# Performance work log

Hardware: AMD Instinct MI355X
Metric: run time of the kernel (lower is better)

The kernel has to match this reference:

```python
import jax, jax.numpy as jnp
import numpy as np

D_MODEL = 256
NUM_HEADS = 8
NUM_KV_HEADS = 4
HEAD_DIM = D_MODEL // NUM_HEADS
EPS = 1e-5


def layer_norm(x, g, b):
    mu = jnp.mean(x, axis=-1, keepdims=True)
    var = jnp.var(x, axis=-1, keepdims=True)
    return (x - mu) * jax.lax.rsqrt(var + EPS) * g + b


def gqa(x_q, x_kv, Wq, bq, Wk, bk, Wv, bv, Wo, bo):
    # x_q, x_kv: [BC, S, D]
    BC, S, D = x_q.shape
    G = NUM_HEADS // NUM_KV_HEADS
    q = (x_q @ Wq + bq).reshape(BC, S, NUM_HEADS, HEAD_DIM)
    k = (x_kv @ Wk + bk).reshape(BC, S, NUM_KV_HEADS, HEAD_DIM)
    v = (x_kv @ Wv + bv).reshape(BC, S, NUM_KV_HEADS, HEAD_DIM)
    # repeat_interleave over head dim to expand KV heads to query heads
    k = jnp.repeat(k, G, axis=2)
    v = jnp.repeat(v, G, axis=2)
    scale = 1.0 / np.sqrt(HEAD_DIM).astype(np.float32)
    scores = jnp.einsum('bqhd,bkhd->bhqk', q, k) * scale  # [BC,H,S,S]
    attn = jax.nn.softmax(scores, axis=-1)
    out = jnp.einsum('bhqk,bkhd->bqhd', attn, v).reshape(BC, S, D)
    return out @ Wo + bo


def _make_params(key):
    ks = jax.random.split(key, 20)
    D, Dkv = D_MODEL, NUM_KV_HEADS * HEAD_DIM
    s = 1.0 / np.sqrt(D).astype(np.float32)
    p = {}
    # 4 LayerNorms
    for name in ['spec_q', 'spec_kv', 'spat_q', 'spat_kv']:
        p[f'ln_{name}_g'] = jnp.ones((D,), jnp.float32)
        p[f'ln_{name}_b'] = jnp.zeros((D,), jnp.float32)
    # two GQA modules: s2t and t2s
    i = 0
    for tag in ['s2t', 't2s']:
        p[f'Wq_{tag}'] = jax.random.normal(ks[i], (D, D), jnp.float32) * s; i += 1
        p[f'bq_{tag}'] = jnp.zeros((D,), jnp.float32)
        p[f'Wk_{tag}'] = jax.random.normal(ks[i], (D, Dkv), jnp.float32) * s; i += 1
        p[f'bk_{tag}'] = jnp.zeros((Dkv,), jnp.float32)
        p[f'Wv_{tag}'] = jax.random.normal(ks[i], (D, Dkv), jnp.float32) * s; i += 1
        p[f'bv_{tag}'] = jnp.zeros((Dkv,), jnp.float32)
        p[f'Wo_{tag}'] = jax.random.normal(ks[i], (D, D), jnp.float32) * s; i += 1
        p[f'bo_{tag}'] = jnp.zeros((D,), jnp.float32)
    p['gate_spec'] = jnp.zeros((1,), jnp.float32)
    p['gate_spat'] = jnp.zeros((1,), jnp.float32)
    return p


def setup_inputs() -> dict:
    key = jax.random.key(0)
    k1, k2, k3 = jax.random.split(key, 3)
    B, S, C, D = 8, 64, 128, D_MODEL
    inp = {
        'x_spec': jax.random.normal(k1, (B, S, C, D), jnp.float32),
        'x_spat': jax.random.normal(k2, (B, S, C, D), jnp.float32),
    }
    inp.update(_make_params(k3))
    return inp


def reference(x_spec, x_spat,
              ln_spec_q_g, ln_spec_q_b, ln_spec_kv_g, ln_spec_kv_b,
              ln_spat_q_g, ln_spat_q_b, ln_spat_kv_g, ln_spat_kv_b,
              Wq_s2t, bq_s2t, Wk_s2t, bk_s2t, Wv_s2t, bv_s2t, Wo_s2t, bo_s2t,
              Wq_t2s, bq_t2s, Wk_t2s, bk_t2s, Wv_t2s, bv_t2s, Wo_t2s, bo_t2s,
              gate_spec, gate_spat):
    B, S, C, D = x_spec.shape
    # (B,S,C,D) -> (B*C, S, D)
    spec_flat = jnp.transpose(x_spec, (0, 2, 1, 3)).reshape(B * C, S, D)
    spat_flat = jnp.transpose(x_spat, (0, 2, 1, 3)).reshape(B * C, S, D)

    spec_q = layer_norm(spec_flat, ln_spec_q_g, ln_spec_q_b)
    spat_kv = layer_norm(spat_flat, ln_spat_kv_g, ln_spat_kv_b)
    delta_spec = gqa(spec_q, spat_kv, Wq_s2t, bq_s2t, Wk_s2t, bk_s2t, Wv_s2t, bv_s2t, Wo_s2t, bo_s2t)

    spat_q = layer_norm(spat_flat, ln_spat_q_g, ln_spat_q_b)
    spec_kv = layer_norm(spec_flat, ln_spec_kv_g, ln_spec_kv_b)
    delta_spat = gqa(spat_q, spec_kv, Wq_t2s, bq_t2s, Wk_t2s, bk_t2s, Wv_t2s, bv_t2s, Wo_t2s, bo_t2s)

    delta_spec = jnp.transpose(delta_spec.reshape(B, C, S, D), (0, 2, 1, 3))
    delta_spat = jnp.transpose(delta_spat.reshape(B, C, S, D), (0, 2, 1, 3))

    out_spec = x_spec + jax.nn.sigmoid(gate_spec) * delta_spec
    out_spat = x_spat + jax.nn.sigmoid(gate_spat) * delta_spat
    return (out_spec, out_spat)
```

## Files before the change

kernel.cpp:

```cpp
#include <hip/hip_runtime.h>

typedef short short8 __attribute__((ext_vector_type(8)));
typedef float f32x4 __attribute__((ext_vector_type(4)));

#define NELT 16777216

__device__ __forceinline__ float b2f(unsigned short u) {
    return __uint_as_float(((unsigned)u) << 16);
}
__device__ __forceinline__ unsigned short f2b(float f) {
    unsigned u = __float_as_uint(f);
    u += 0x7FFF + ((u >> 16) & 1);
    return (unsigned short)(u >> 16);
}
__device__ __forceinline__ void split2(float f, unsigned short& hi, unsigned short& lo) {
    unsigned short h = f2b(f);
    hi = h;
    lo = f2b(f - b2f(h));
}
__device__ __forceinline__ int xrow_off(int r) {
    int n = r >> 6, s = r & 63;
    int b = n >> 7, c = n & 127;
    return (((b << 6) + s) * 128 + c) << 8;
}
__device__ __forceinline__ int sw256(int row, int k) {
    return row * 256 + ((((k >> 3) ^ (row & 7)) << 3) | (k & 7));
}
__device__ __forceinline__ int boff(int nt, int kk, int ct, int lq, int lm) {
    return ((((nt * 8 + kk) * 4 + ct) * 4 + lq) * 16 + lm) * 16;
}

__global__ __launch_bounds__(256) void w_prep(
    const float* __restrict__ Wq, const float* __restrict__ Wk,
    const float* __restrict__ Wv, const float* __restrict__ Wo,
    unsigned short* __restrict__ Bqkv, unsigned short* __restrict__ Bo)
{
    const int tid = blockIdx.x * 256 + threadIdx.x;
    const int lm = tid & 15, lq = (tid >> 4) & 3, ct = (tid >> 6) & 3;
    const int kk = (tid >> 8) & 7, nt = tid >> 11;
    const int c = ct * 16 + lm;
    {
        const float* W; int ldw, col;
        if (nt < 4)      { W = Wq; ldw = 256; col = nt * 64 + c; }
        else if (nt < 6) { W = Wk; ldw = 128; col = (nt - 4) * 64 + c; }
        else             { W = Wv; ldw = 128; col = (nt - 6) * 64 + c; }
        short8 h8, l8;
        #pragma unroll
        for (int j = 0; j < 8; ++j) {
            int k = kk * 32 + lq * 8 + j;
            unsigned short h, l;
            split2(W[k * ldw + col], h, l);
            h8[j] = (short)h; l8[j] = (short)l;
        }
        int off = boff(nt, kk, ct, lq, lm);
        *(short8*)&Bqkv[off] = h8;
        *(short8*)&Bqkv[off + 8] = l8;
    }
    if (nt < 4) {
        int col = nt * 64 + c;
        short8 h8, l8;
        #pragma unroll
        for (int j = 0; j < 8; ++j) {
            int k = kk * 32 + lq * 8 + j;
            unsigned short h, l;
            split2(Wo[k * 256 + col], h, l);
            h8[j] = (short)h; l8[j] = (short)l;
        }
        int off = boff(nt, kk, ct, lq, lm);
        *(short8*)&Bo[off] = h8;
        *(short8*)&Bo[off + 8] = l8;
    }
}

struct FusedArgs {
    const float* xq[2];   const float* xkv[2];
    const float* gq[2];   const float* btq[2];
    const float* gkv[2];  const float* btkv[2];
    const unsigned short* Bqkv[2];
    const unsigned short* Bow[2];
    const float* bq[2];   const float* bk[2];
    const float* bv[2];   const float* bo[2];
    const float* gate[2];
    float* out[2];
};

__global__ __launch_bounds__(256, 2) void fused(FusedArgs P_)
{
    __shared__ char SM[65536];
    unsigned short* Ah = (unsigned short*)SM;
    unsigned short* Al = (unsigned short*)(SM + 32768);
    const int dir = blockIdx.y;
    const int n = blockIdx.x, t = threadIdx.x;
    const int r0 = n * 64;
    const int w = t >> 6, l = t & 63, lm = l & 15, lq = l >> 4;
    unsigned short* slot = (unsigned short*)(SM + w * 16384);

    const float* xq  = P_.xq[dir];
    const float* xkv = P_.xkv[dir];
    const unsigned short* Bq  = P_.Bqkv[dir];
    const unsigned short* BoW = P_.Bow[dir];

    auto stage = [&](const float* X, const float* G, const float* BT) {
        float4 xv[16];
        #pragma unroll
        for (int it = 0; it < 16; ++it)
            xv[it] = *(const float4*)(X + xrow_off(r0 + it * 4 + w) + l * 4);
        const float4 gv = *(const float4*)(G + l * 4);
        const float4 b4 = *(const float4*)(BT + l * 4);
        #pragma unroll
        for (int it = 0; it < 16; ++it) {
            int row = it * 4 + w;
            float4 x4 = xv[it];
            float s1 = x4.x + x4.y + x4.z + x4.w;
            float s2 = x4.x * x4.x + x4.y * x4.y + x4.z * x4.z + x4.w * x4.w;
            #pragma unroll
            for (int m = 1; m < 64; m <<= 1) {
                s1 += __shfl_xor(s1, m);
                s2 += __shfl_xor(s2, m);
            }
            float mu = s1 * (1.f / 256.f);
            float rstd = rsqrtf(s2 * (1.f / 256.f) - mu * mu + 1e-5f);
            float v0 = (x4.x - mu) * rstd * gv.x + b4.x;
            float v1 = (x4.y - mu) * rstd * gv.y + b4.y;
            float v2 = (x4.z - mu) * rstd * gv.z + b4.z;
            float v3 = (x4.w - mu) * rstd * gv.w + b4.w;
            ushort4 oh, ol;
            split2(v0, oh.x, ol.x); split2(v1, oh.y, ol.y);
            split2(v2, oh.z, ol.z); split2(v3, oh.w, ol.w);
            *(ushort4*)&Ah[sw256(row, l * 4)] = oh;
            *(ushort4*)&Al[sw256(row, l * 4)] = ol;
        }
    };

    stage(xkv, P_.gkv[dir], P_.btkv[dir]);
    __syncthreads();

    f32x4 kacc[4][2] = {};
    f32x4 vacc[4][2] = {};
    {
        const int ntK = 4 + (w >> 1), ntV = 6 + (w >> 1);
        #pragma unroll
        for (int kk = 0; kk < 8; ++kk) {
            int k0 = kk * 32 + lq * 8;
            short8 ah[4], al[4];
            #pragma unroll
            for (int m = 0; m < 4; ++m) {
                ah[m] = *(const short8*)&Ah[sw256(m * 16 + lm, k0)];
                al[m] = *(const short8*)&Al[sw256(m * 16 + lm, k0)];
            }
            #pragma unroll
            for (int i = 0; i < 2; ++i) {
                int ct = (2 * w + i) & 3;
                int offK = boff(ntK, kk, ct, lq, lm);
                short8 bh = *(const short8*)&Bq[offK];
                short8 bl = *(const short8*)&Bq[offK + 8];
                #pragma unroll
                for (int m = 0; m < 4; ++m) {
                    kacc[m][i] = __builtin_amdgcn_mfma_f32_16x16x32_bf16(ah[m], bh, kacc[m][i], 0, 0, 0);
                    kacc[m][i] = __builtin_amdgcn_mfma_f32_16x16x32_bf16(al[m], bh, kacc[m][i], 0, 0, 0);
                    kacc[m][i] = __builtin_amdgcn_mfma_f32_16x16x32_bf16(ah[m], bl, kacc[m][i], 0, 0, 0);
                }
                int offV = boff(ntV, kk, ct, lq, lm);
                bh = *(const short8*)&Bq[offV];
                bl = *(const short8*)&Bq[offV + 8];
                #pragma unroll
                for (int m = 0; m < 4; ++m) {
                    vacc[m][i] = __builtin_amdgcn_mfma_f32_16x16x32_bf16(ah[m], bh, vacc[m][i], 0, 0, 0);
                    vacc[m][i] = __builtin_amdgcn_mfma_f32_16x16x32_bf16(al[m], bh, vacc[m][i], 0, 0, 0);
                    vacc[m][i] = __builtin_amdgcn_mfma_f32_16x16x32_bf16(ah[m], bl, vacc[m][i], 0, 0, 0);
                }
            }
        }
    }
    __syncthreads();

    unsigned short* Ks = slot;
    unsigned short* Vs = slot + 2560;
    {
        float bkv0 = P_.bk[dir][w * 32 + lm],  bkv1 = P_.bk[dir][w * 32 + 16 + lm];
        float bvv0 = P_.bv[dir][w * 32 + lm],  bvv1 = P_.bv[dir][w * 32 + 16 + lm];
        #pragma unroll
        for (int m = 0; m < 4; ++m) {
            #pragma unroll
            for (int rg = 0; rg < 4; ++rg) {
                int key = m * 16 + lq * 4 + rg;
                Ks[key * 40 + lm]      = f2b(kacc[m][0][rg] + bkv0);
                Ks[key * 40 + 16 + lm] = f2b(kacc[m][1][rg] + bkv1);
                Vs[lm * 72 + key]        = f2b(vacc[m][0][rg] + bvv0);
                Vs[(16 + lm) * 72 + key] = f2b(vacc[m][1][rg] + bvv1);
            }
        }
    }
    short8 kf[4];
    #pragma unroll
    for (int nt = 0; nt < 4; ++nt)
        kf[nt] = *(const short8*)&Ks[(nt * 16 + lm) * 40 + lq * 8];
    short8 vb[2][2];
    #pragma unroll
    for (int kt = 0; kt < 2; ++kt) {
        vb[kt][0] = *(const short8*)&Vs[lm * 72 + kt * 32 + lq * 8];
        vb[kt][1] = *(const short8*)&Vs[(16 + lm) * 72 + kt * 32 + lq * 8];
    }
    __syncthreads();

    stage(xq, P_.gq[dir], P_.btq[dir]);
    __syncthreads();

    f32x4 qacc[4][4] = {};
    #pragma unroll
    for (int kk = 0; kk < 8; ++kk) {
        int k0 = kk * 32 + lq * 8;
        short8 ah[4], al[4];
        #pragma unroll
        for (int m = 0; m < 4; ++m) {
            ah[m] = *(const short8*)&Ah[sw256(m * 16 + lm, k0)];
            al[m] = *(const short8*)&Al[sw256(m * 16 + lm, k0)];
        }
        #pragma unroll
        for (int i = 0; i < 4; ++i) {
            int off = boff(w, kk, i, lq, lm);
            short8 bh = *(const short8*)&Bq[off];
            short8 bl = *(const short8*)&Bq[off + 8];
            #pragma unroll
            for (int m = 0; m < 4; ++m) {
                qacc[m][i] = __builtin_amdgcn_mfma_f32_16x16x32_bf16(ah[m], bh, qacc[m][i], 0, 0, 0);
                qacc[m][i] = __builtin_amdgcn_mfma_f32_16x16x32_bf16(al[m], bh, qacc[m][i], 0, 0, 0);
                qacc[m][i] = __builtin_amdgcn_mfma_f32_16x16x32_bf16(ah[m], bl, qacc[m][i], 0, 0, 0);
            }
        }
    }
    __syncthreads();

    unsigned short* Qs = slot;
    {
        float bq0 = P_.bq[dir][w * 64 + lm],      bq1 = P_.bq[dir][w * 64 + 16 + lm];
        float bq2 = P_.bq[dir][w * 64 + 32 + lm], bq3 = P_.bq[dir][w * 64 + 48 + lm];
        #pragma unroll
        for (int m = 0; m < 4; ++m) {
            #pragma unroll
            for (int rg = 0; rg < 4; ++rg) {
                int row = (m * 16 + lq * 4 + rg) * 72;
                Qs[row + lm]      = f2b(qacc[m][0][rg] + bq0);
                Qs[row + 16 + lm] = f2b(qacc[m][1][rg] + bq1);
                Qs[row + 32 + lm] = f2b(qacc[m][2][rg] + bq2);
                Qs[row + 48 + lm] = f2b(qacc[m][3][rg] + bq3);
            }
        }
    }
    short8 qf[2][4];
    #pragma unroll
    for (int hi = 0; hi < 2; ++hi)
        #pragma unroll
        for (int mt = 0; mt < 4; ++mt)
            qf[hi][mt] = *(const short8*)&Qs[(mt * 16 + lm) * 72 + hi * 32 + lq * 8];

    unsigned short* Pw = slot;
    const float scale = 0.17677669529663687f;
    f32x4 o[2][4][2] = {};
    #pragma unroll
    for (int hi = 0; hi < 2; ++hi) {
        f32x4 s[4][4];
        #pragma unroll
        for (int mt = 0; mt < 4; ++mt) {
            #pragma unroll
            for (int nt = 0; nt < 4; ++nt) {
                f32x4 z = {0, 0, 0, 0};
                s[mt][nt] = __builtin_amdgcn_mfma_f32_16x16x32_bf16(qf[hi][mt], kf[nt], z, 0, 0, 0);
            }
        }
        #pragma unroll
        for (int mt = 0; mt < 4; ++mt) {
            #pragma unroll
            for (int rg = 0; rg < 4; ++rg) {
                float mx = fmaxf(fmaxf(s[mt][0][rg], s[mt][1][rg]),
                                 fmaxf(s[mt][2][rg], s[mt][3][rg]));
                #pragma unroll
                for (int msk = 1; msk < 16; msk <<= 1)
                    mx = fmaxf(mx, __shfl_xor(mx, msk));
                float p0 = __expf((s[mt][0][rg] - mx) * scale);
                float p1 = __expf((s[mt][1][rg] - mx) * scale);
                float p2 = __expf((s[mt][2][rg] - mx) * scale);
                float p3 = __expf((s[mt][3][rg] - mx) * scale);
                float sum = p0 + p1 + p2 + p3;
                #pragma unroll
                for (int msk = 1; msk < 16; msk <<= 1)
                    sum += __shfl_xor(sum, msk);
                float inv = 1.f / sum;
                int rowb = (mt * 16 + lq * 4 + rg) * 72 + lm;
                Pw[rowb + 0]  = f2b(p0 * inv);
                Pw[rowb + 16] = f2b(p1 * inv);
                Pw[rowb + 32] = f2b(p2 * inv);
                Pw[rowb + 48] = f2b(p3 * inv);
            }
        }
        #pragma unroll
        for (int kt = 0; kt < 2; ++kt) {
            #pragma unroll
            for (int mt = 0; mt < 4; ++mt) {
                short8 pa = *(const short8*)&Pw[(mt * 16 + lm) * 72 + kt * 32 + lq * 8];
                o[hi][mt][0] = __builtin_amdgcn_mfma_f32_16x16x32_bf16(pa, vb[kt][0], o[hi][mt][0], 0, 0, 0);
                o[hi][mt][1] = __builtin_amdgcn_mfma_f32_16x16x32_bf16(pa, vb[kt][1], o[hi][mt][1], 0, 0, 0);
            }
        }
    }
    __syncthreads();

    #pragma unroll
    for (int hi = 0; hi < 2; ++hi) {
        #pragma unroll
        for (int mt = 0; mt < 4; ++mt) {
            #pragma unroll
            for (int n2 = 0; n2 < 2; ++n2) {
                #pragma unroll
                for (int rg = 0; rg < 4; ++rg) {
                    int row = mt * 16 + lq * 4 + rg;
                    int col = w * 64 + hi * 32 + n2 * 16 + lm;
                    unsigned short h_, l_;
                    split2(o[hi][mt][n2][rg], h_, l_);
                    int sw = sw256(row, col);
                    Ah[sw] = h_;
                    Al[sw] = l_;
                }
            }
        }
    }
    __syncthreads();

    f32x4 acc[4][4] = {};
    #pragma unroll
    for (int kk = 0; kk < 8; ++kk) {
        int k0 = kk * 32 + lq * 8;
        short8 ah[4], al[4];
        #pragma unroll
        for (int m = 0; m < 4; ++m) {
            ah[m] = *(const short8*)&Ah[sw256(m * 16 + lm, k0)];
            al[m] = *(const short8*)&Al[sw256(m * 16 + lm, k0)];
        }
        #pragma unroll
        for (int i = 0; i < 4; ++i) {
            int off = boff(w, kk, i, lq, lm);
            short8 bh = *(const short8*)&BoW[off];
            short8 bl = *(const short8*)&BoW[off + 8];
            #pragma unroll
            for (int m = 0; m < 4; ++m) {
                acc[m][i] = __builtin_amdgcn_mfma_f32_16x16x32_bf16(ah[m], bh, acc[m][i], 0, 0, 0);
                acc[m][i] = __builtin_amdgcn_mfma_f32_16x16x32_bf16(al[m], bh, acc[m][i], 0, 0, 0);
                acc[m][i] = __builtin_amdgcn_mfma_f32_16x16x32_bf16(ah[m], bl, acc[m][i], 0, 0, 0);
            }
        }
    }
    float sig = 1.f / (1.f + __expf(-P_.gate[dir][0]));
    const float* Xres = xq;
    float* Out = P_.out[dir];
    #pragma unroll
    for (int i = 0; i < 4; ++i) {
        int col = w * 64 + i * 16 + lm;
        float bias = P_.bo[dir][col];
        #pragma unroll
        for (int m = 0; m < 4; ++m) {
            #pragma unroll
            for (int rg = 0; rg < 4; ++rg) {
                int row = m * 16 + lq * 4 + rg;
                int oidx = xrow_off(r0 + row) + col;
                Out[oidx] = Xres[oidx] + sig * (acc[m][i][rg] + bias);
            }
        }
    }
}

extern "C" void kernel_launch(void* const* d_in, const int* in_sizes, int n_in,
                              void* d_out, int out_size, void* d_ws, size_t ws_size,
                              hipStream_t stream) {
    const float* x_spec = (const float*)d_in[0];
    const float* x_spat = (const float*)d_in[1];
    const float* ln_g[4] = {(const float*)d_in[2], (const float*)d_in[4],
                            (const float*)d_in[6], (const float*)d_in[8]};
    const float* ln_b[4] = {(const float*)d_in[3], (const float*)d_in[5],
                            (const float*)d_in[7], (const float*)d_in[9]};
    char* ws = (char*)d_ws;
    unsigned short* Bqkv[2] = {(unsigned short*)ws,
                               (unsigned short*)(ws + (512 << 10))};
    unsigned short* BoL[2]  = {(unsigned short*)(ws + (1024 << 10)),
                               (unsigned short*)(ws + (1280 << 10))};

    for (int dir = 0; dir < 2; ++dir) {
        int base = 10 + dir * 8;
        w_prep<<<64, 256, 0, stream>>>(
            (const float*)d_in[base + 0], (const float*)d_in[base + 2],
            (const float*)d_in[base + 4], (const float*)d_in[base + 6],
            Bqkv[dir], BoL[dir]);
    }

    FusedArgs A;
    for (int dir = 0; dir < 2; ++dir) {
        int base = 10 + dir * 8;
        A.xq[dir]   = dir == 0 ? x_spec : x_spat;
        A.xkv[dir]  = dir == 0 ? x_spat : x_spec;
        A.gq[dir]   = dir == 0 ? ln_g[0] : ln_g[2];
        A.btq[dir]  = dir == 0 ? ln_b[0] : ln_b[2];
        A.gkv[dir]  = dir == 0 ? ln_g[3] : ln_g[1];
        A.btkv[dir] = dir == 0 ? ln_b[3] : ln_b[1];
        A.Bqkv[dir] = Bqkv[dir];
        A.Bow[dir]  = BoL[dir];
        A.bq[dir]   = (const float*)d_in[base + 1];
        A.bk[dir]   = (const float*)d_in[base + 3];
        A.bv[dir]   = (const float*)d_in[base + 5];
        A.bo[dir]   = (const float*)d_in[base + 7];
        A.gate[dir] = (const float*)d_in[26 + dir];
        A.out[dir]  = (float*)d_out + (size_t)dir * NELT;
    }
    fused<<<dim3(1024, 2), 256, 0, stream>>>(A);
}
```

Measured before the change: 534.4 us.

## Halve LDS staging buffer to raise occupancy; merge weight-prep launches

The LDS A-operand buffer shrinks from 64 KB to 40 KB by staging and multiplying the 64-row tile in two 32-row halves for the K/V, Q and output projections. Launch bounds go from 2 to 4 blocks per CU so more waves can hide latency. The cost is extra __syncthreads and more passes over the weight fragments. The two per-direction w_prep launches are also merged into one 2D-grid launch to cut launch overhead.

Measured after the change: 660.2 us. +23.5%, slower.

```diff
diff --git a/kernel.cpp b/kernel.cpp
--- a/kernel.cpp
+++ b/kernel.cpp
@@ -30,20 +30,22 @@
     return ((((nt * 8 + kk) * 4 + ct) * 4 + lq) * 16 + lm) * 16;
 }
 
-__global__ __launch_bounds__(256) void w_prep(
-    const float* __restrict__ Wq, const float* __restrict__ Wk,
-    const float* __restrict__ Wv, const float* __restrict__ Wo,
-    unsigned short* __restrict__ Bqkv, unsigned short* __restrict__ Bo)
+struct WArgs {
+    const float* Wq[2]; const float* Wk[2]; const float* Wv[2]; const float* Wo[2];
+    unsigned short* Bqkv[2]; unsigned short* Bo[2];
+};
+__global__ __launch_bounds__(256) void w_prep(WArgs A)
 {
+    const int dir = blockIdx.y;
     const int tid = blockIdx.x * 256 + threadIdx.x;
     const int lm = tid & 15, lq = (tid >> 4) & 3, ct = (tid >> 6) & 3;
     const int kk = (tid >> 8) & 7, nt = tid >> 11;
     const int c = ct * 16 + lm;
     {
         const float* W; int ldw, col;
-        if (nt < 4)      { W = Wq; ldw = 256; col = nt * 64 + c; }
-        else if (nt < 6) { W = Wk; ldw = 128; col = (nt - 4) * 64 + c; }
-        else             { W = Wv; ldw = 128; col = (nt - 6) * 64 + c; }
+        if (nt < 4)      { W = A.Wq[dir]; ldw = 256; col = nt * 64 + c; }
+        else if (nt < 6) { W = A.Wk[dir]; ldw = 128; col = (nt - 4) * 64 + c; }
+        else             { W = A.Wv[dir]; ldw = 128; col = (nt - 6) * 64 + c; }
         short8 h8, l8;
         #pragma unroll
         for (int j = 0; j < 8; ++j) {
@@ -53,8 +55,8 @@
             h8[j] = (short)h; l8[j] = (short)l;
         }
         int off = boff(nt, kk, ct, lq, lm);
-        *(short8*)&Bqkv[off] = h8;
-        *(short8*)&Bqkv[off + 8] = l8;
+        *(short8*)&A.Bqkv[dir][off] = h8;
+        *(short8*)&A.Bqkv[dir][off + 8] = l8;
     }
     if (nt < 4) {
         int col = nt * 64 + c;
@@ -63,12 +65,12 @@
         for (int j = 0; j < 8; ++j) {
             int k = kk * 32 + lq * 8 + j;
             unsigned short h, l;
-            split2(Wo[k * 256 + col], h, l);
+            split2(A.Wo[dir][k * 256 + col], h, l);
             h8[j] = (short)h; l8[j] = (short)l;
         }
         int off = boff(nt, kk, ct, lq, lm);
-        *(short8*)&Bo[off] = h8;
-        *(short8*)&Bo[off + 8] = l8;
+        *(short8*)&A.Bo[dir][off] = h8;
+        *(short8*)&A.Bo[dir][off + 8] = l8;
     }
 }
 
@@ -84,31 +86,29 @@
     float* out[2];
 };
 
-__global__ __launch_bounds__(256, 2) void fused(FusedArgs P_)
+__global__ __launch_bounds__(256, 4) void fused(FusedArgs P_)
 {
-    __shared__ char SM[65536];
+    __shared__ char SM[40960];
     unsigned short* Ah = (unsigned short*)SM;
-    unsigned short* Al = (unsigned short*)(SM + 32768);
+    unsigned short* Al = (unsigned short*)(SM + 16384);
     const int dir = blockIdx.y;
     const int n = blockIdx.x, t = threadIdx.x;
     const int r0 = n * 64;
     const int w = t >> 6, l = t & 63, lm = l & 15, lq = l >> 4;
-    unsigned short* slot = (unsigned short*)(SM + w * 16384);
+    unsigned short* slot = (unsigned short*)(SM + w * 10240);
 
     const float* xq  = P_.xq[dir];
     const float* xkv = P_.xkv[dir];
     const unsigned short* Bq  = P_.Bqkv[dir];
     const unsigned short* BoW = P_.Bow[dir];
 
-    auto stage = [&](const float* X, const float* G, const float* BT) {
-        float4 xv[16];
-        #pragma unroll
-        for (int it = 0; it < 16; ++it)
-            xv[it] = *(const float4*)(X + xrow_off(r0 + it * 4 + w) + l * 4);
-        const float4 gv = *(const float4*)(G + l * 4);
-        const float4 b4 = *(const float4*)(BT + l * 4);
-        #pragma unroll
-        for (int it = 0; it < 16; ++it) {
+    auto stage_half = [&](const float* X, const float4& gv, const float4& b4, int h) {
+        float4 xv[8];
+        #pragma unroll
+        for (int it = 0; it < 8; ++it)
+            xv[it] = *(const float4*)(X + xrow_off(r0 + h * 32 + it * 4 + w) + l * 4);
+        #pragma unroll
+        for (int it = 0; it < 8; ++it) {
             int row = it * 4 + w;
             float4 x4 = xv[it];
             float s1 = x4.x + x4.y + x4.z + x4.w;
@@ -132,47 +132,53 @@
         }
     };
 
-    stage(xkv, P_.gkv[dir], P_.btkv[dir]);
-    __syncthreads();
-
     f32x4 kacc[4][2] = {};
     f32x4 vacc[4][2] = {};
     {
+        const float4 gv = *(const float4*)(P_.gkv[dir] + l * 4);
+        const float4 b4 = *(const float4*)(P_.btkv[dir] + l * 4);
         const int ntK = 4 + (w >> 1), ntV = 6 + (w >> 1);
         #pragma unroll
-        for (int kk = 0; kk < 8; ++kk) {
-            int k0 = kk * 32 + lq * 8;
-            short8 ah[4], al[4];
-            #pragma unroll
-            for (int m = 0; m < 4; ++m) {
-                ah[m] = *(const short8*)&Ah[sw256(m * 16 + lm, k0)];
-                al[m] = *(const short8*)&Al[sw256(m * 16 + lm, k0)];
-            }
-            #pragma unroll
-            for (int i = 0; i < 2; ++i) {
-                int ct = (2 * w + i) & 3;
-                int offK = boff(ntK, kk, ct, lq, lm);
-                short8 bh = *(const short8*)&Bq[offK];
-                short8 bl = *(const short8*)&Bq[offK + 8];
-                #pragma unroll
-                for (int m = 0; m < 4; ++m) {
-                    kacc[m][i] = __builtin_amdgcn_mfma_f32_16x16x32_bf16(ah[m], bh, kacc[m][i], 0, 0, 0);
-                    kacc[m][i] = __builtin_amdgcn_mfma_f32_16x16x32_bf16(al[m], bh, kacc[m][i], 0, 0, 0);
-                    kacc[m][i] = __builtin_amdgcn_mfma_f32_16x16x32_bf16(ah[m], bl, kacc[m][i], 0, 0, 0);
-                }
-                int offV = boff(ntV, kk, ct, lq, lm);
-                bh = *(const short8*)&Bq[offV];
-                bl = *(const short8*)&Bq[offV + 8];
-                #pragma unroll
-                for (int m = 0; m < 4; ++m) {
-                    vacc[m][i] = __builtin_amdgcn_mfma_f32_16x16x32_bf16(ah[m], bh, vacc[m][i], 0, 0, 0);
-                    vacc[m][i] = __builtin_amdgcn_mfma_f32_16x16x32_bf16(al[m], bh, vacc[m][i], 0, 0, 0);
-                    vacc[m][i] = __builtin_amdgcn_mfma_f32_16x16x32_bf16(ah[m], bl, vacc[m][i], 0, 0, 0);
-                }
-            }
-        }
-    }
-    __syncthreads();
+        for (int h = 0; h < 2; ++h) {
+            stage_half(xkv, gv, b4, h);
+            __syncthreads();
+            #pragma unroll
+            for (int kk = 0; kk < 8; ++kk) {
+                int k0 = kk * 32 + lq * 8;
+                short8 ah[2], al[2];
+                #pragma unroll
+                for (int m2 = 0; m2 < 2; ++m2) {
+                    ah[m2] = *(const short8*)&Ah[sw256(m2 * 16 + lm, k0)];
+                    al[m2] = *(const short8*)&Al[sw256(m2 * 16 + lm, k0)];
+                }
+                #pragma unroll
+                for (int i = 0; i < 2; ++i) {
+                    int ct = (2 * w + i) & 3;
+                    int offK = boff(ntK, kk, ct, lq, lm);
+                    short8 bh = *(const short8*)&Bq[offK];
+                    short8 bl = *(const short8*)&Bq[offK + 8];
+                    #pragma unroll
+                    for (int m2 = 0; m2 < 2; ++m2) {
+                        int m = 2 * h + m2;
+                        kacc[m][i] = __builtin_amdgcn_mfma_f32_16x16x32_bf16(ah[m2], bh, kacc[m][i], 0, 0, 0);
+                        kacc[m][i] = __builtin_amdgcn_mfma_f32_16x16x32_bf16(al[m2], bh, kacc[m][i], 0, 0, 0);
+                        kacc[m][i] = __builtin_amdgcn_mfma_f32_16x16x32_bf16(ah[m2], bl, kacc[m][i], 0, 0, 0);
+                    }
+                    int offV = boff(ntV, kk, ct, lq, lm);
+                    bh = *(const short8*)&Bq[offV];
+                    bl = *(const short8*)&Bq[offV + 8];
+                    #pragma unroll
+                    for (int m2 = 0; m2 < 2; ++m2) {
+                        int m = 2 * h + m2;
+                        vacc[m][i] = __builtin_amdgcn_mfma_f32_16x16x32_bf16(ah[m2], bh, vacc[m][i], 0, 0, 0);
+                        vacc[m][i] = __builtin_amdgcn_mfma_f32_16x16x32_bf16(al[m2], bh, vacc[m][i], 0, 0, 0);
+                        vacc[m][i] = __builtin_amdgcn_mfma_f32_16x16x32_bf16(ah[m2], bl, vacc[m][i], 0, 0, 0);
+                    }
+                }
+            }
+            __syncthreads();
+        }
+    }
 
     unsigned short* Ks = slot;
     unsigned short* Vs = slot + 2560;
@@ -203,33 +209,40 @@
     }
     __syncthreads();
 
-    stage(xq, P_.gq[dir], P_.btq[dir]);
-    __syncthreads();
-
     f32x4 qacc[4][4] = {};
-    #pragma unroll
-    for (int kk = 0; kk < 8; ++kk) {
-        int k0 = kk * 32 + lq * 8;
-        short8 ah[4], al[4];
-        #pragma unroll
-        for (int m = 0; m < 4; ++m) {
-            ah[m] = *(const short8*)&Ah[sw256(m * 16 + lm, k0)];
-            al[m] = *(const short8*)&Al[sw256(m * 16 + lm, k0)];
-        }
-        #pragma unroll
-        for (int i = 0; i < 4; ++i) {
-            int off = boff(w, kk, i, lq, lm);
-            short8 bh = *(const short8*)&Bq[off];
-            short8 bl = *(const short8*)&Bq[off + 8];
-            #pragma unroll
-            for (int m = 0; m < 4; ++m) {
-                qacc[m][i] = __builtin_amdgcn_mfma_f32_16x16x32_bf16(ah[m], bh, qacc[m][i], 0, 0, 0);
-                qacc[m][i] = __builtin_amdgcn_mfma_f32_16x16x32_bf16(al[m], bh, qacc[m][i], 0, 0, 0);
-                qacc[m][i] = __builtin_amdgcn_mfma_f32_16x16x32_bf16(ah[m], bl, qacc[m][i], 0, 0, 0);
-            }
-        }
-    }
-    __syncthreads();
+    {
+        const float4 gv = *(const float4*)(P_.gq[dir] + l * 4);
+        const float4 b4 = *(const float4*)(P_.btq[dir] + l * 4);
+        #pragma unroll
+        for (int h = 0; h < 2; ++h) {
+            stage_half(xq, gv, b4, h);
+            __syncthreads();
+            #pragma unroll
+            for (int kk = 0; kk < 8; ++kk) {
+                int k0 = kk * 32 + lq * 8;
+                short8 ah[2], al[2];
+                #pragma unroll
+                for (int m2 = 0; m2 < 2; ++m2) {
+                    ah[m2] = *(const short8*)&Ah[sw256(m2 * 16 + lm, k0)];
+                    al[m2] = *(const short8*)&Al[sw256(m2 * 16 + lm, k0)];
+                }
+                #pragma unroll
+                for (int i = 0; i < 4; ++i) {
+                    int off = boff(w, kk, i, lq, lm);
+                    short8 bh = *(const short8*)&Bq[off];
+                    short8 bl = *(const short8*)&Bq[off + 8];
+                    #pragma unroll
+                    for (int m2 = 0; m2 < 2; ++m2) {
+                        int m = 2 * h + m2;
+                        qacc[m][i] = __builtin_amdgcn_mfma_f32_16x16x32_bf16(ah[m2], bh, qacc[m][i], 0, 0, 0);
+                        qacc[m][i] = __builtin_amdgcn_mfma_f32_16x16x32_bf16(al[m2], bh, qacc[m][i], 0, 0, 0);
+                        qacc[m][i] = __builtin_amdgcn_mfma_f32_16x16x32_bf16(ah[m2], bl, qacc[m][i], 0, 0, 0);
+                    }
+                }
+            }
+            __syncthreads();
+        }
+    }
 
     unsigned short* Qs = slot;
     {
@@ -305,49 +318,54 @@
     }
     __syncthreads();
 
-    #pragma unroll
-    for (int hi = 0; hi < 2; ++hi) {
-        #pragma unroll
-        for (int mt = 0; mt < 4; ++mt) {
-            #pragma unroll
-            for (int n2 = 0; n2 < 2; ++n2) {
-                #pragma unroll
-                for (int rg = 0; rg < 4; ++rg) {
-                    int row = mt * 16 + lq * 4 + rg;
-                    int col = w * 64 + hi * 32 + n2 * 16 + lm;
-                    unsigned short h_, l_;
-                    split2(o[hi][mt][n2][rg], h_, l_);
-                    int sw = sw256(row, col);
-                    Ah[sw] = h_;
-                    Al[sw] = l_;
-                }
-            }
-        }
-    }
-    __syncthreads();
-
     f32x4 acc[4][4] = {};
     #pragma unroll
-    for (int kk = 0; kk < 8; ++kk) {
-        int k0 = kk * 32 + lq * 8;
-        short8 ah[4], al[4];
-        #pragma unroll
-        for (int m = 0; m < 4; ++m) {
-            ah[m] = *(const short8*)&Ah[sw256(m * 16 + lm, k0)];
-            al[m] = *(const short8*)&Al[sw256(m * 16 + lm, k0)];
-        }
-        #pragma unroll
-        for (int i = 0; i < 4; ++i) {
-            int off = boff(w, kk, i, lq, lm);
-            short8 bh = *(const short8*)&BoW[off];
-            short8 bl = *(const short8*)&BoW[off + 8];
-            #pragma unroll
-            for (int m = 0; m < 4; ++m) {
-                acc[m][i] = __builtin_amdgcn_mfma_f32_16x16x32_bf16(ah[m], bh, acc[m][i], 0, 0, 0);
-                acc[m][i] = __builtin_amdgcn_mfma_f32_16x16x32_bf16(al[m], bh, acc[m][i], 0, 0, 0);
-                acc[m][i] = __builtin_amdgcn_mfma_f32_16x16x32_bf16(ah[m], bl, acc[m][i], 0, 0, 0);
-            }
-        }
+    for (int h = 0; h < 2; ++h) {
+        #pragma unroll
+        for (int m2 = 0; m2 < 2; ++m2) {
+            int mt = 2 * h + m2;
+            #pragma unroll
+            for (int hi = 0; hi < 2; ++hi) {
+                #pragma unroll
+                for (int n2 = 0; n2 < 2; ++n2) {
+                    #pragma unroll
+                    for (int rg = 0; rg < 4; ++rg) {
+                        int row = m2 * 16 + lq * 4 + rg;
+                        int col = w * 64 + hi * 32 + n2 * 16 + lm;
+                        unsigned short h_, l_;
+                        split2(o[hi][mt][n2][rg], h_, l_);
+                        int sw = sw256(row, col);
+                        Ah[sw] = h_;
+                        Al[sw] = l_;
+                    }
+                }
+            }
+        }
+        __syncthreads();
+        #pragma unroll
+        for (int kk = 0; kk < 8; ++kk) {
+            int k0 = kk * 32 + lq * 8;
+            short8 ah[2], al[2];
+            #pragma unroll
+            for (int m2 = 0; m2 < 2; ++m2) {
+                ah[m2] = *(const short8*)&Ah[sw256(m2 * 16 + lm, k0)];
+                al[m2] = *(const short8*)&Al[sw256(m2 * 16 + lm, k0)];
+            }
+            #pragma unroll
+            for (int i = 0; i < 4; ++i) {
+                int off = boff(w, kk, i, lq, lm);
+                short8 bh = *(const short8*)&BoW[off];
+                short8 bl = *(const short8*)&BoW[off + 8];
+                #pragma unroll
+                for (int m2 = 0; m2 < 2; ++m2) {
+                    int m = 2 * h + m2;
+                    acc[m][i] = __builtin_amdgcn_mfma_f32_16x16x32_bf16(ah[m2], bh, acc[m][i], 0, 0, 0);
+                    acc[m][i] = __builtin_amdgcn_mfma_f32_16x16x32_bf16(al[m2], bh, acc[m][i], 0, 0, 0);
+                    acc[m][i] = __builtin_amdgcn_mfma_f32_16x16x32_bf16(ah[m2], bl, acc[m][i], 0, 0, 0);
+                }
+            }
+        }
+        __syncthreads();
     }
     float sig = 1.f / (1.f + __expf(-P_.gate[dir][0]));
     const float* Xres = xq;
@@ -383,13 +401,17 @@
     unsigned short* BoL[2]  = {(unsigned short*)(ws + (1024 << 10)),
                                (unsigned short*)(ws + (1280 << 10))};
 
+    WArgs WA;
     for (int dir = 0; dir < 2; ++dir) {
         int base = 10 + dir * 8;
-        w_prep<<<64, 256, 0, stream>>>(
-            (const float*)d_in[base + 0], (const float*)d_in[base + 2],
-            (const float*)d_in[base + 4], (const float*)d_in[base + 6],
-            Bqkv[dir], BoL[dir]);
-    }
+        WA.Wq[dir] = (const float*)d_in[base + 0];
+        WA.Wk[dir] = (const float*)d_in[base + 2];
+        WA.Wv[dir] = (const float*)d_in[base + 4];
+        WA.Wo[dir] = (const float*)d_in[base + 6];
+        WA.Bqkv[dir] = Bqkv[dir];
+        WA.Bo[dir]   = BoL[dir];
+    }
+    w_prep<<<dim3(64, 2), 256, 0, stream>>>(WA);
 
     FusedArgs A;
     for (int dir = 0; dir < 2; ++dir) {
```
